# Kernel tuning notes

Measured on AMD Instinct MI355X. Metric: run time of the kernel, lower is better.

## Reference

```python
import jax, jax.numpy as jnp
import numpy as np

B, S, E, H = 8, 1024, 512, 8
NEG = -1e10


def setup_inputs() -> dict:
    key = jax.random.key(0)
    ks = jax.random.split(key, 8)
    k = jax.random.normal(ks[0], (B, S, E), dtype=jnp.float32)
    v = jax.random.normal(ks[1], (B, S, E), dtype=jnp.float32)
    q = jax.random.normal(ks[2], (B, S, E), dtype=jnp.float32)
    # causal mask, broadcastable like torch masked_fill
    mask = jnp.tril(jnp.ones((S, S), dtype=jnp.int32))[None, None]
    sc = 1.0 / np.sqrt(E)
    Wk = jax.random.normal(ks[3], (H * E, E), dtype=jnp.float32) * sc
    Wq = jax.random.normal(ks[4], (H * E, E), dtype=jnp.float32) * sc
    Wv = jax.random.normal(ks[5], (H * E, E), dtype=jnp.float32) * sc
    Wo = jax.random.normal(ks[6], (E, H * E), dtype=jnp.float32) * (1.0 / np.sqrt(H * E))
    bo = jnp.zeros((E,), dtype=jnp.float32)
    return {"k": k, "v": v, "q": q, "mask": mask,
            "Wk": Wk, "Wq": Wq, "Wv": Wv, "Wo": Wo, "bo": bo}


def reference(k, v, q, mask, Wk, Wq, Wv, Wo, bo):
    b, q_len, e = q.shape
    k_len, v_len = k.shape[1], v.shape[1]
    h = Wk.shape[0] // e
    scale = jnp.sqrt(jnp.asarray(e // h, dtype=jnp.float32))
    # projections E -> H*E (torch Linear: x @ W.T)
    wk = (k @ Wk.T).reshape(b, h, k_len, e)   # raw reshape, matches torch .view
    wq = (q @ Wq.T).reshape(b, h, q_len, e)
    wv = (v @ Wv.T).reshape(b, h, v_len, e)
    energy = jnp.einsum('bhqe,bhke->bhqk', wq, wk)
    energy = jnp.where(mask == 0, NEG, energy)  # mask applied BEFORE scaling, as in source
    energy = energy / scale
    attn = jax.nn.softmax(energy, axis=-1)
    f = jnp.einsum('bhqk,bhke->bhqe', attn, wv)
    f = jnp.transpose(f, (0, 2, 1, 3)).reshape(b, q_len, h * e)
    return f @ Wo.T + bo
```

## Files before the change

kernel.cpp:

```cpp
#include <hip/hip_runtime.h>


typedef _Float16 half8 __attribute__((ext_vector_type(8)));
typedef _Float16 half4v __attribute__((ext_vector_type(4)));
typedef float f32x4 __attribute__((ext_vector_type(4)));

typedef __attribute__((address_space(3))) unsigned int lds_u32_t;
typedef __attribute__((address_space(1))) unsigned int g_u32_t;

__device__ __forceinline__ void glds16(const void* g, void* l) {
  __builtin_amdgcn_global_load_lds((const g_u32_t*)g, (lds_u32_t*)l, 16, 0, 0);
}

template <int HL>
__device__ __forceinline__ void gemm_core(const _Float16* A, const _Float16* B,
                                          int lda, int ldb, int kmax,
                                          long sAh, long sBh,
                                          _Float16* As, _Float16* Bs,
                                          f32x4 (&acc)[4][4]) {
  int tid = (int)threadIdx.x;
  int w = tid >> 6, lane = tid & 63;
  int wr = (w >> 1) * 64, wc = (w & 1) * 64;
  int lr = lane & 15, lk = (lane >> 4) * 8;
  int srow = lane >> 2, sseg = (lane & 3) * 8;

  for (int h = 0; h < HL; h++) {
    const _Float16* Ah = A + (size_t)h * sAh;
    const _Float16* Bh = B + (size_t)h * sBh;
    for (int k0 = 0; k0 < kmax; k0 += 64) {
      __syncthreads();
#pragma unroll
      for (int p = 0; p < 2; p++)
#pragma unroll
        for (int t = 0; t < 2; t++) {
          glds16(Ah + (size_t)(w * 32 + t * 16 + srow) * lda + k0 + p * 32 + sseg,
                 As + p * 4096 + (w * 32 + t * 16) * 32);
          glds16(Bh + (size_t)(w * 32 + t * 16 + srow) * ldb + k0 + p * 32 + sseg,
                 Bs + p * 4096 + (w * 32 + t * 16) * 32);
        }
      __syncthreads();
#pragma unroll
      for (int p = 0; p < 2; p++) {
        half8 a[4], b[4];
#pragma unroll
        for (int mi = 0; mi < 4; mi++)
          a[mi] = *(half8*)&As[p * 4096 + (wr + mi * 16 + lr) * 32 + lk];
#pragma unroll
        for (int ni = 0; ni < 4; ni++)
          b[ni] = *(half8*)&Bs[p * 4096 + (wc + ni * 16 + lr) * 32 + lk];
#pragma unroll
        for (int mi = 0; mi < 4; mi++)
#pragma unroll
          for (int ni = 0; ni < 4; ni++)
            acc[mi][ni] =
                __builtin_amdgcn_mfma_f32_16x16x32_f16(a[mi], b[ni], acc[mi][ni], 0, 0, 0);
      }
    }
  }
}

__device__ __forceinline__ void epilogue_f16(f32x4 (&acc)[4][4], _Float16* T,
                                             _Float16* Cp, size_t cOff,
                                             int i0, int j0, int ldc) {
  int tid = (int)threadIdx.x;
  int w = tid >> 6, lane = tid & 63;
  int wr = (w >> 1) * 64, wc = (w & 1) * 64;
  int r0 = (lane >> 4) * 4, col = lane & 15;
  __syncthreads();
#pragma unroll
  for (int mi = 0; mi < 4; mi++)
#pragma unroll
    for (int ni = 0; ni < 4; ni++)
#pragma unroll
      for (int r = 0; r < 4; r++)
        T[(size_t)(wr + mi * 16 + r0 + r) * 136 + wc + ni * 16 + col] =
            (_Float16)acc[mi][ni][r];
  __syncthreads();
#pragma unroll
  for (int s = 0; s < 8; s++) {
    int row = w * 32 + s * 4 + (lane >> 4);
    int c8 = (lane & 15) * 8;
    half8 h = *(half8*)&T[(size_t)row * 136 + c8];
    *(half8*)(Cp + cOff + (size_t)(i0 + row) * ldc + j0 + c8) = h;
  }
}

__device__ __forceinline__ void epilogue_atomic(f32x4 (&acc)[4][4], float* Cp,
                                                size_t cOff, int i0, int j0, int ldc) {
  int tid = (int)threadIdx.x;
  int w = tid >> 6, lane = tid & 63;
  int wr = (w >> 1) * 64, wc = (w & 1) * 64;
  int r0 = (lane >> 4) * 4, col = lane & 15;
#pragma unroll
  for (int mi = 0; mi < 4; mi++)
#pragma unroll
    for (int ni = 0; ni < 4; ni++)
#pragma unroll
      for (int r = 0; r < 4; r++)
        unsafeAtomicAdd(Cp + cOff + (size_t)(i0 + wr + mi * 16 + r0 + r) * ldc +
                            j0 + wc + ni * 16 + col,
                        acc[mi][ni][r]);
}

template <int HG>
__global__ __launch_bounds__(256) void proj_kernel(const _Float16* __restrict__ in16,
                                                   const _Float16* __restrict__ W16,
                                                   _Float16* __restrict__ Qp,
                                                   _Float16* __restrict__ Kp,
                                                   _Float16* __restrict__ Vp) {
  __shared__ __align__(16) _Float16 smem[17408];
  int x = (int)blockIdx.x, Y = (int)blockIdx.y, Z = (int)blockIdx.z;
  int i0 = (x >> 5) * 128, j0 = (x & 31) * 128;
  const _Float16* A = in16 + (size_t)Y * HG * 524288 + (size_t)Z * HG * 65536 +
                      (size_t)i0 * 512;
  const _Float16* B = W16 + (size_t)Y * 2097152 + (size_t)j0 * 512;
  _Float16* C = (Y == 0 ? Qp : (Y == 1 ? Kp : Vp));
  f32x4 acc[4][4] = {};
  gemm_core<1>(A, B, 512, 512, 512, 0, 0, smem, smem + 8192, acc);
  epilogue_f16(acc, smem, C, (size_t)Z * HG * 524288, i0, j0, 4096);
}

template <int HG>
__global__ __launch_bounds__(256) void vwo_kernel(const _Float16* __restrict__ Vp,
                                                  const _Float16* __restrict__ WoG,
                                                  _Float16* __restrict__ VWo) {
  __shared__ __align__(16) _Float16 smem[17408];
  int x = (int)blockIdx.x, Y = (int)blockIdx.y, Z = (int)blockIdx.z;
  size_t z = (size_t)Z * HG + Y;
  int i0 = (x >> 3) * 128, j0 = (x & 7) * 128;
  const _Float16* A = WoG + (size_t)Y * 512 + (size_t)i0 * 4096;
  const _Float16* B = Vp + z * 524288 + (size_t)j0 * 512;
  f32x4 acc[4][4] = {};
  gemm_core<1>(A, B, 4096, 512, 512, 0, 0, smem, smem + 8192, acc);
  epilogue_f16(acc, smem, VWo, z * 524288, i0, j0, 1024);
}

template <int HG>
__global__ __launch_bounds__(256) void energy_kernel(const _Float16* __restrict__ Qp,
                                                     const _Float16* __restrict__ Kp,
                                                     _Float16* __restrict__ E) {
  __shared__ __align__(16) _Float16 smem[17408];
  int x = (int)blockIdx.x, Y = (int)blockIdx.y, Z = (int)blockIdx.z;
  size_t z = (size_t)Z * HG + Y;
  int ti = (int)((sqrtf(8.0f * x + 1.0f) - 1.0f) * 0.5f);
  if (ti * (ti + 1) / 2 > x) ti--;
  else if ((ti + 1) * (ti + 2) / 2 <= x) ti++;
  int tj = x - ti * (ti + 1) / 2;
  int i0 = ti * 128, j0 = tj * 128;
  const _Float16* A = Qp + z * 524288 + (size_t)i0 * 512;
  const _Float16* B = Kp + z * 524288 + (size_t)j0 * 512;
  f32x4 acc[4][4] = {};
  gemm_core<1>(A, B, 512, 512, 512, 0, 0, smem, smem + 8192, acc);
  epilogue_f16(acc, smem, E, z * 1048576, i0, j0, 1024);
}

template <int HG, int HL>
__global__ __launch_bounds__(256) void pv_kernel(const _Float16* __restrict__ E,
                                                 const _Float16* __restrict__ VWo,
                                                 float* __restrict__ out) {
  __shared__ __align__(16) _Float16 smem[17408];
  int x = (int)blockIdx.x, Y = (int)blockIdx.y, Z = (int)blockIdx.z;
  int i0 = (x >> 2) * 128, j0 = (x & 3) * 128;
  int kmax = i0 + 128;
  const _Float16* A = E + ((size_t)Z * HG + (size_t)Y * HL) * 1048576 + (size_t)i0 * 1024;
  const _Float16* B = VWo + ((size_t)Z * HG + (size_t)Y * HL) * 524288 + (size_t)j0 * 1024;
  f32x4 acc[4][4] = {};
  gemm_core<HL>(A, B, 1024, 1024, kmax, 1048576, 524288, smem, smem + 8192, acc);
  epilogue_atomic(acc, out, (size_t)Z * 524288, i0, j0, 512);
}

__global__ __launch_bounds__(256) void softmax_rows(void* __restrict__ Ep) {
  int R = (int)blockIdx.x * 4 + ((int)threadIdx.x >> 6);
  int lane = (int)threadIdx.x & 63;
  int i = R & 1023;
  int nt = (i >> 8) + 1;
  _Float16* row = (_Float16*)Ep + (size_t)R * 1024;
  float x[16];
  float m = -3.0e38f;
#pragma unroll
  for (int t = 0; t < 4; t++) {
    if (t < nt) {
      int j0 = t * 256 + lane * 4;
      half4v h = *(const half4v*)(row + j0);
#pragma unroll
      for (int c = 0; c < 4; c++) {
        float v = (j0 + c <= i) ? (float)h[c] * 0.125f : -3.0e38f;
        x[t * 4 + c] = v;
        m = fmaxf(m, v);
      }
    }
  }
#pragma unroll
  for (int s = 32; s > 0; s >>= 1) m = fmaxf(m, __shfl_xor(m, s, 64));
  float p[16];
  float sum = 0.0f;
#pragma unroll
  for (int t = 0; t < 4; t++) {
    if (t < nt) {
#pragma unroll
      for (int c = 0; c < 4; c++) {
        p[t * 4 + c] = exp2f((x[t * 4 + c] - m) * 1.44269504f);
        sum += p[t * 4 + c];
      }
    }
  }
#pragma unroll
  for (int s = 32; s > 0; s >>= 1) sum += __shfl_xor(sum, s, 64);
  float inv = 1.0f / sum;
#pragma unroll
  for (int t = 0; t < 4; t++) {
    if (t < nt) {
      int j0 = t * 256 + lane * 4;
      half4v h;
#pragma unroll
      for (int c = 0; c < 4; c++) h[c] = (_Float16)(p[t * 4 + c] * inv);
      *(half4v*)(row + j0) = h;
    }
  }
}

__global__ __launch_bounds__(256) void wbconv(const float* __restrict__ Wq,
                                              const float* __restrict__ Wk,
                                              const float* __restrict__ Wv,
                                              const float* __restrict__ Wo,
                                              _Float16* __restrict__ W16,
                                              float* __restrict__ out,
                                              const float* __restrict__ bo) {
  int bx = (int)blockIdx.x;
  if (bx < 4096) {
    size_t base = ((size_t)bx * 256 + threadIdx.x) * 8;
    int wid = (int)(base >> 21);
    size_t off = base & 2097151;
    const float* src = wid == 0 ? Wq : (wid == 1 ? Wk : (wid == 2 ? Wv : Wo));
    float4 a = *(const float4*)(src + off);
    float4 b = *(const float4*)(src + off + 4);
    half8 h;
    h[0] = (_Float16)a.x; h[1] = (_Float16)a.y; h[2] = (_Float16)a.z; h[3] = (_Float16)a.w;
    h[4] = (_Float16)b.x; h[5] = (_Float16)b.y; h[6] = (_Float16)b.z; h[7] = (_Float16)b.w;
    *(half8*)(W16 + base) = h;
  } else {
    size_t idx = ((size_t)(bx - 4096) * 256 + threadIdx.x) * 4;
    *(float4*)(out + idx) = *(const float4*)(bo + (idx & 511));
  }
}

template <int HG>
__global__ __launch_bounds__(256) void inconv(const float* __restrict__ q,
                                              const float* __restrict__ k,
                                              const float* __restrict__ v,
                                              _Float16* __restrict__ dst) {
  int Y = (int)blockIdx.y;
  size_t base = ((size_t)blockIdx.x * 256 + threadIdx.x) * 8;
  size_t b = base / (HG * 65536);
  size_t within = base - b * (HG * 65536);
  const float* src = (Y == 0 ? q : (Y == 1 ? k : v)) + b * 524288 + within;
  float4 a = ((const float4*)src)[0];
  float4 c = ((const float4*)src)[1];
  half8 h;
  h[0] = (_Float16)a.x; h[1] = (_Float16)a.y; h[2] = (_Float16)a.z; h[3] = (_Float16)a.w;
  h[4] = (_Float16)c.x; h[5] = (_Float16)c.y; h[6] = (_Float16)c.z; h[7] = (_Float16)c.w;
  *(half8*)(dst + (size_t)Y * HG * 524288 + base) = h;
}

template <int HG>
static void run_pipeline(const float* q_in, const float* k_in, const float* v_in,
                         const float* Wq, const float* Wk, const float* Wv,
                         const float* Wo, const float* bo, float* out, char* ws,
                         hipStream_t stream) {
  const int NG = 8 / HG;
  const long zc = 8 * HG;
  _Float16* W16 = (_Float16*)ws;
  _Float16* in16 = W16 + 8388608;
  _Float16* Qp = in16 + 3L * HG * 524288;
  _Float16* Kp = Qp + zc * 524288;
  _Float16* VWo = Kp + zc * 524288;
  _Float16* E = VWo + zc * 524288;
  _Float16* Vp = E;
  _Float16* Wo16 = W16 + 3 * 2097152;
  dim3 blk(256);

  wbconv<<<dim3(8192), blk, 0, stream>>>(Wq, Wk, Wv, Wo, W16, out, bo);

  constexpr int HL = (HG >= 2) ? 2 : 1;
  constexpr int YS = HG / HL;

  for (int g = 0; g < NG; g++) {
    inconv<HG><<<dim3(HG * 256, 3), blk, 0, stream>>>(
        q_in + (size_t)g * HG * 65536, k_in + (size_t)g * HG * 65536,
        v_in + (size_t)g * HG * 65536, in16);

    proj_kernel<HG><<<dim3(HG * 32, 3, 8), blk, 0, stream>>>(in16, W16, Qp, Kp, Vp);

    vwo_kernel<HG><<<dim3(32, HG, 8), blk, 0, stream>>>(
        Vp, Wo16 + (size_t)g * HG * 512, VWo);

    energy_kernel<HG><<<dim3(36, HG, 8), blk, 0, stream>>>(Qp, Kp, E);

    softmax_rows<<<dim3(zc * 256), blk, 0, stream>>>(E);

    pv_kernel<HG, HL><<<dim3(32, YS, 8), blk, 0, stream>>>(E, VWo, out);
  }
}

extern "C" void kernel_launch(void* const* d_in, const int* in_sizes, int n_in,
                              void* d_out, int out_size, void* d_ws, size_t ws_size,
                              hipStream_t stream) {
  const float* k_in = (const float*)d_in[0];
  const float* v_in = (const float*)d_in[1];
  const float* q_in = (const float*)d_in[2];
  const float* Wk = (const float*)d_in[4];
  const float* Wq = (const float*)d_in[5];
  const float* Wv = (const float*)d_in[6];
  const float* Wo = (const float*)d_in[7];
  const float* bo = (const float*)d_in[8];
  float* out = (float*)d_out;
  char* ws = (char*)d_ws;

  if (ws_size >= (size_t)197132288)
    run_pipeline<4>(q_in, k_in, v_in, Wq, Wk, Wv, Wo, bo, out, ws, stream);
  else if (ws_size >= (size_t)106954752)
    run_pipeline<2>(q_in, k_in, v_in, Wq, Wk, Wv, Wo, bo, out, ws, stream);
  else
    run_pipeline<1>(q_in, k_in, v_in, Wq, Wk, Wv, Wo, bo, out, ws, stream);
}
```

Baseline: 579.7 us.

## Replace 128x128 GEMMs with 256x256-tile, 4-stage async LDS pipelined kernels

Projection, V·Wo and energy GEMMs move from 128x128 tiles with 256 threads to 256x256 tiles with 512 threads. Each block uses a 4-buffer global_load_lds pipeline with XOR-swizzled LDS, explicit vmcnt waits and setprio around the MFMA block. A swizzled per-wave LDS epilogue replaces the old one. The goal is more data reuse per tile and better overlap of loads with MFMA. In exchange, the kernels use 128KB of LDS per block and far more accumulator registers, and launch fewer blocks (causal energy gets only 10 tiles per head), which risks lower occupancy and poorer load balance.

```diff
diff --git a/kernel.cpp b/kernel.cpp
--- a/kernel.cpp
+++ b/kernel.cpp
@@ -10,6 +10,153 @@
 
 __device__ __forceinline__ void glds16(const void* g, void* l) {
   __builtin_amdgcn_global_load_lds((const g_u32_t*)g, (lds_u32_t*)l, 16, 0, 0);
+}
+
+__device__ __forceinline__ void stage_panel(const _Float16* __restrict__ G,
+                                            int ld, _Float16* Ls, int tid) {
+  int w = tid >> 6;
+#pragma unroll
+  for (int e = 0; e < 2; e++) {
+    int X = e * 8192 + tid * 16;
+    int r = X >> 6;
+    int s = (X >> 4) & 3;
+    glds16(G + (size_t)r * ld + ((s ^ (r & 3)) << 3),
+           Ls + ((e * 8192 + w * 1024) >> 1));
+  }
+}
+
+template <int NT>
+__device__ __forceinline__ void gemm256_core(const _Float16* __restrict__ A,
+                                             const _Float16* __restrict__ B,
+                                             int lda, int ldb,
+                                             _Float16* smem, f32x4 (&acc)[8][4]) {
+  int tid = (int)threadIdx.x;
+  int w = tid >> 6, lane = tid & 63;
+  int wr = (w >> 2) * 128, wc = (w & 3) * 64;
+  int lr = lane & 15;
+  int sw = ((lane >> 4) ^ (lane & 3)) << 3;
+
+#pragma unroll
+  for (int t = 0; t < 3; t++) {
+    if (t < NT) {
+      stage_panel(A + t * 32, lda, smem + t * 16384, tid);
+      stage_panel(B + t * 32, ldb, smem + t * 16384 + 8192, tid);
+    }
+  }
+  for (int t = 0; t < NT; t++) {
+    if (t + 3 < NT) {
+      _Float16* buf = smem + ((t + 3) & 3) * 16384;
+      stage_panel(A + (t + 3) * 32, lda, buf, tid);
+      stage_panel(B + (t + 3) * 32, ldb, buf + 8192, tid);
+    }
+    int ahead = NT - 1 - t;
+    if (ahead > 3) ahead = 3;
+    if (ahead == 3)      asm volatile("s_waitcnt vmcnt(12)" ::: "memory");
+    else if (ahead == 2) asm volatile("s_waitcnt vmcnt(8)" ::: "memory");
+    else if (ahead == 1) asm volatile("s_waitcnt vmcnt(4)" ::: "memory");
+    else                 asm volatile("s_waitcnt vmcnt(0)" ::: "memory");
+    __builtin_amdgcn_s_barrier();
+    __builtin_amdgcn_sched_barrier(0);
+    const _Float16* As = smem + (t & 3) * 16384;
+    const _Float16* Bs = As + 8192;
+    half8 a[8], b[4];
+#pragma unroll
+    for (int ni = 0; ni < 4; ni++)
+      b[ni] = *(const half8*)&Bs[(wc + ni * 16 + lr) * 32 + sw];
+#pragma unroll
+    for (int mi = 0; mi < 8; mi++)
+      a[mi] = *(const half8*)&As[(wr + mi * 16 + lr) * 32 + sw];
+    __builtin_amdgcn_s_setprio(1);
+#pragma unroll
+    for (int mi = 0; mi < 8; mi++)
+#pragma unroll
+      for (int ni = 0; ni < 4; ni++)
+        acc[mi][ni] = __builtin_amdgcn_mfma_f32_16x16x32_f16(a[mi], b[ni],
+                                                             acc[mi][ni], 0, 0, 0);
+    __builtin_amdgcn_s_setprio(0);
+    __builtin_amdgcn_sched_barrier(0);
+    __builtin_amdgcn_s_barrier();
+  }
+}
+
+__device__ __forceinline__ void epilogue256(f32x4 (&acc)[8][4], _Float16* lds,
+                                            _Float16* Cp, size_t cOff,
+                                            int i0, int j0, int ldc) {
+  int tid = (int)threadIdx.x;
+  int w = tid >> 6, lane = tid & 63;
+  int wr = (w >> 2) * 128, wc = (w & 3) * 64;
+  int r0 = (lane >> 4) * 4, cl = lane & 15;
+  _Float16* T = lds + w * 8192;
+#pragma unroll
+  for (int mi = 0; mi < 8; mi++)
+#pragma unroll
+    for (int ni = 0; ni < 4; ni++) {
+      int colb = ni * 16 + cl;
+#pragma unroll
+      for (int r = 0; r < 4; r++) {
+        int row = mi * 16 + r0 + r;
+        T[row * 64 + ((((colb >> 3) ^ row) & 7) << 3) + (colb & 7)] =
+            (_Float16)acc[mi][ni][r];
+      }
+    }
+#pragma unroll
+  for (int st = 0; st < 16; st++) {
+    int row = st * 8 + (lane >> 3);
+    int c8 = lane & 7;
+    half8 h = *(const half8*)&T[row * 64 + (((c8 ^ row) & 7) << 3)];
+    *(half8*)(Cp + cOff + (size_t)(i0 + wr + row) * ldc + j0 + wc + c8 * 8) = h;
+  }
+}
+
+template <int HG>
+__global__ __launch_bounds__(512, 2) void proj256(const _Float16* __restrict__ in16,
+                                                  const _Float16* __restrict__ W16,
+                                                  _Float16* __restrict__ Qp,
+                                                  _Float16* __restrict__ Kp,
+                                                  _Float16* __restrict__ Vp) {
+  __shared__ __align__(16) _Float16 smem[65536];
+  int x = (int)blockIdx.x, Y = (int)blockIdx.y;
+  int it = x >> 4, jt = x & 15;
+  const _Float16* A = in16 + (size_t)Y * HG * 524288 + (size_t)it * 131072;
+  const _Float16* B = W16 + (size_t)Y * 2097152 + (size_t)jt * 131072;
+  _Float16* C = (Y == 0 ? Qp : (Y == 1 ? Kp : Vp));
+  f32x4 acc[8][4] = {};
+  gemm256_core<16>(A, B, 512, 512, smem, acc);
+  epilogue256(acc, smem, C, 0, it * 256, jt * 256, 4096);
+}
+
+template <int HG>
+__global__ __launch_bounds__(512, 2) void vwo256(const _Float16* __restrict__ Vp,
+                                                 const _Float16* __restrict__ WoG,
+                                                 _Float16* __restrict__ VWo) {
+  __shared__ __align__(16) _Float16 smem[65536];
+  int x = (int)blockIdx.x, Y = (int)blockIdx.y, Z = (int)blockIdx.z;
+  size_t z = (size_t)Z * HG + Y;
+  int i0 = (x >> 2) * 256, j0 = (x & 3) * 256;
+  const _Float16* A = WoG + (size_t)Y * 512 + (size_t)i0 * 4096;
+  const _Float16* B = Vp + z * 524288 + (size_t)j0 * 512;
+  f32x4 acc[8][4] = {};
+  gemm256_core<16>(A, B, 4096, 512, smem, acc);
+  epilogue256(acc, smem, VWo, z * 524288, i0, j0, 1024);
+}
+
+template <int HG>
+__global__ __launch_bounds__(512, 2) void energy256(const _Float16* __restrict__ Qp,
+                                                    const _Float16* __restrict__ Kp,
+                                                    _Float16* __restrict__ E) {
+  __shared__ __align__(16) _Float16 smem[65536];
+  int x = (int)blockIdx.x, Y = (int)blockIdx.y, Z = (int)blockIdx.z;
+  size_t z = (size_t)Z * HG + Y;
+  int ti = (int)((sqrtf(8.0f * x + 1.0f) - 1.0f) * 0.5f);
+  if (ti * (ti + 1) / 2 > x) ti--;
+  else if ((ti + 1) * (ti + 2) / 2 <= x) ti++;
+  int tj = x - ti * (ti + 1) / 2;
+  int i0 = ti * 256, j0 = tj * 256;
+  const _Float16* A = Qp + z * 524288 + (size_t)i0 * 512;
+  const _Float16* B = Kp + z * 524288 + (size_t)j0 * 512;
+  f32x4 acc[8][4] = {};
+  gemm256_core<16>(A, B, 512, 512, smem, acc);
+  epilogue256(acc, smem, E, z * 1048576, i0, j0, 1024);
 }
 
 template <int HL>
@@ -59,32 +206,6 @@
   }
 }
 
-__device__ __forceinline__ void epilogue_f16(f32x4 (&acc)[4][4], _Float16* T,
-                                             _Float16* Cp, size_t cOff,
-                                             int i0, int j0, int ldc) {
-  int tid = (int)threadIdx.x;
-  int w = tid >> 6, lane = tid & 63;
-  int wr = (w >> 1) * 64, wc = (w & 1) * 64;
-  int r0 = (lane >> 4) * 4, col = lane & 15;
-  __syncthreads();
-#pragma unroll
-  for (int mi = 0; mi < 4; mi++)
-#pragma unroll
-    for (int ni = 0; ni < 4; ni++)
-#pragma unroll
-      for (int r = 0; r < 4; r++)
-        T[(size_t)(wr + mi * 16 + r0 + r) * 136 + wc + ni * 16 + col] =
-            (_Float16)acc[mi][ni][r];
-  __syncthreads();
-#pragma unroll
-  for (int s = 0; s < 8; s++) {
-    int row = w * 32 + s * 4 + (lane >> 4);
-    int c8 = (lane & 15) * 8;
-    half8 h = *(half8*)&T[(size_t)row * 136 + c8];
-    *(half8*)(Cp + cOff + (size_t)(i0 + row) * ldc + j0 + c8) = h;
-  }
-}
-
 __device__ __forceinline__ void epilogue_atomic(f32x4 (&acc)[4][4], float* Cp,
                                                 size_t cOff, int i0, int j0, int ldc) {
   int tid = (int)threadIdx.x;
@@ -100,58 +221,6 @@
         unsafeAtomicAdd(Cp + cOff + (size_t)(i0 + wr + mi * 16 + r0 + r) * ldc +
                             j0 + wc + ni * 16 + col,
                         acc[mi][ni][r]);
-}
-
-template <int HG>
-__global__ __launch_bounds__(256) void proj_kernel(const _Float16* __restrict__ in16,
-                                                   const _Float16* __restrict__ W16,
-                                                   _Float16* __restrict__ Qp,
-                                                   _Float16* __restrict__ Kp,
-                                                   _Float16* __restrict__ Vp) {
-  __shared__ __align__(16) _Float16 smem[17408];
-  int x = (int)blockIdx.x, Y = (int)blockIdx.y, Z = (int)blockIdx.z;
-  int i0 = (x >> 5) * 128, j0 = (x & 31) * 128;
-  const _Float16* A = in16 + (size_t)Y * HG * 524288 + (size_t)Z * HG * 65536 +
-                      (size_t)i0 * 512;
-  const _Float16* B = W16 + (size_t)Y * 2097152 + (size_t)j0 * 512;
-  _Float16* C = (Y == 0 ? Qp : (Y == 1 ? Kp : Vp));
-  f32x4 acc[4][4] = {};
-  gemm_core<1>(A, B, 512, 512, 512, 0, 0, smem, smem + 8192, acc);
-  epilogue_f16(acc, smem, C, (size_t)Z * HG * 524288, i0, j0, 4096);
-}
-
-template <int HG>
-__global__ __launch_bounds__(256) void vwo_kernel(const _Float16* __restrict__ Vp,
-                                                  const _Float16* __restrict__ WoG,
-                                                  _Float16* __restrict__ VWo) {
-  __shared__ __align__(16) _Float16 smem[17408];
-  int x = (int)blockIdx.x, Y = (int)blockIdx.y, Z = (int)blockIdx.z;
-  size_t z = (size_t)Z * HG + Y;
-  int i0 = (x >> 3) * 128, j0 = (x & 7) * 128;
-  const _Float16* A = WoG + (size_t)Y * 512 + (size_t)i0 * 4096;
-  const _Float16* B = Vp + z * 524288 + (size_t)j0 * 512;
-  f32x4 acc[4][4] = {};
-  gemm_core<1>(A, B, 4096, 512, 512, 0, 0, smem, smem + 8192, acc);
-  epilogue_f16(acc, smem, VWo, z * 524288, i0, j0, 1024);
-}
-
-template <int HG>
-__global__ __launch_bounds__(256) void energy_kernel(const _Float16* __restrict__ Qp,
-                                                     const _Float16* __restrict__ Kp,
-                                                     _Float16* __restrict__ E) {
-  __shared__ __align__(16) _Float16 smem[17408];
-  int x = (int)blockIdx.x, Y = (int)blockIdx.y, Z = (int)blockIdx.z;
-  size_t z = (size_t)Z * HG + Y;
-  int ti = (int)((sqrtf(8.0f * x + 1.0f) - 1.0f) * 0.5f);
-  if (ti * (ti + 1) / 2 > x) ti--;
-  else if ((ti + 1) * (ti + 2) / 2 <= x) ti++;
-  int tj = x - ti * (ti + 1) / 2;
-  int i0 = ti * 128, j0 = tj * 128;
-  const _Float16* A = Qp + z * 524288 + (size_t)i0 * 512;
-  const _Float16* B = Kp + z * 524288 + (size_t)j0 * 512;
-  f32x4 acc[4][4] = {};
-  gemm_core<1>(A, B, 512, 512, 512, 0, 0, smem, smem + 8192, acc);
-  epilogue_f16(acc, smem, E, z * 1048576, i0, j0, 1024);
 }
 
 template <int HG, int HL>
@@ -278,6 +347,7 @@
   _Float16* Vp = E;
   _Float16* Wo16 = W16 + 3 * 2097152;
   dim3 blk(256);
+  dim3 blk5(512);
 
   wbconv<<<dim3(8192), blk, 0, stream>>>(Wq, Wk, Wv, Wo, W16, out, bo);
 
@@ -289,12 +359,12 @@
         q_in + (size_t)g * HG * 65536, k_in + (size_t)g * HG * 65536,
         v_in + (size_t)g * HG * 65536, in16);
 
-    proj_kernel<HG><<<dim3(HG * 32, 3, 8), blk, 0, stream>>>(in16, W16, Qp, Kp, Vp);
-
-    vwo_kernel<HG><<<dim3(32, HG, 8), blk, 0, stream>>>(
+    proj256<HG><<<dim3(HG * 64, 3), blk5, 0, stream>>>(in16, W16, Qp, Kp, Vp);
+
+    vwo256<HG><<<dim3(8, HG, 8), blk5, 0, stream>>>(
         Vp, Wo16 + (size_t)g * HG * 512, VWo);
 
-    energy_kernel<HG><<<dim3(36, HG, 8), blk, 0, stream>>>(Qp, Kp, E);
+    energy256<HG><<<dim3(10, HG, 8), blk5, 0, stream>>>(Qp, Kp, E);
 
     softmax_rows<<<dim3(zc * 256), blk, 0, stream>>>(E);
 
```

Result: faster. 566.8 us (-2.2%).
